# Kernel tuning notes

Measured on AMD Instinct MI355X. Metric: run time of the kernel, lower is better.

The kernel has to match this reference:

```python
import jax, jax.numpy as jnp
import numpy as np

# (multiplicity, dim=2l+1) per irreducible field, for both input and output
RS = [(8, 1), (8, 3), (8, 5)]
SIZE = 3          # conv kernel spatial size
B_EL = 2          # radial basis elements per (i,j) kernel block
EPS = 1e-5


def _se3_bn_conv(x, weight, bases):
    """Training-mode SE3BatchNorm stats fused into dynamic kernel build + conv3d.
    x: (B, C_in, D, H, W); weight: flat (sum mi*mj*b_el,);
    bases[i][j]: (b_el, di, dj, SIZE, SIZE, SIZE).
    """
    B = x.shape[0]
    means = []    # per scalar (d==1) field: (m,)
    scales = []   # per field: (m,) inverse-std factors
    ix = 0
    for m, d in RS:
        field = x[:, ix:ix + m * d].reshape(B, m, d, -1)
        ix += m * d
        if d == 1:
            mean = jax.lax.stop_gradient(field.mean(axis=-1).mean(axis=0).reshape(-1))
            field = field - mean.reshape(1, m, 1, 1)
            means.append(mean)
        # reduce='mean': sum over d, mean over spatial, mean over batch (detached)
        norm = jax.lax.stop_gradient(jnp.sum(field * field, axis=2).mean(axis=-1).mean(axis=0))
        scales.append((norm + EPS) ** -0.5)

    # Build normalized dynamic kernel blocks and compensating bias
    widx = 0
    row_blocks = []
    bias_parts = []
    for i, (mi, di) in enumerate(RS):
        col_blocks = []
        bia = jnp.zeros((mi * di,), x.dtype)
        imean = 0
        for j, (mj, dj) in enumerate(RS):
            basis = bases[i][j]                     # (b, di, dj, s, s, s)
            b = basis.shape[0]
            w = weight[widx:widx + mi * mj * b].reshape(mi, mj, b)
            widx += mi * mj * b
            w = w * scales[j][None, :, None]        # per-input-field BN rescale
            # block: (mi*di, mj*dj, s, s, s)
            block = jnp.einsum('uvb,bdexyz->udvexyz', w, basis)
            col_blocks.append(block.reshape(mi * di, mj * dj, SIZE, SIZE, SIZE))
            if di == 1 and dj == 1:
                mean = means[imean]
                imean += 1
                identity = basis.reshape(b, -1).sum(-1)         # (b,)
                corr = (w.reshape(-1, b) @ identity[:, None]).reshape(mi, mj)
                bia = bia - (corr @ mean[:, None]).reshape(-1)
        row_blocks.append(jnp.concatenate(col_blocks, axis=1))
        bias_parts.append(bia)
    kernel = jnp.concatenate(row_blocks, axis=0)    # (C_out, C_in, s, s, s)
    bias = jnp.concatenate(bias_parts)              # (C_out,)

    out = jax.lax.conv_general_dilated(
        x, kernel, window_strides=(1, 1, 1), padding='VALID',
        dimension_numbers=('NCDHW', 'OIDHW', 'NCDHW'))
    return out + bias[None, :, None, None, None]


def setup_inputs() -> dict:
    key = jax.random.key(0)
    k_x, k_w = jax.random.split(key)
    C = sum(m * d for m, d in RS)  # 72
    x = jax.random.normal(k_x, (8, C, 32, 32, 32), jnp.float32)
    total_w = sum(mi * mj * B_EL for mi, _ in RS for mj, _ in RS)  # 1152
    weight = jax.random.normal(k_w, (total_w,), jnp.float32) * 0.1
    inp = {'x': x, 'weight': weight}
    for i, (mi, di) in enumerate(RS):
        for j, (mj, dj) in enumerate(RS):
            kb = jax.random.fold_in(key, 100 + 10 * i + j)
            inp['basis_{}_{}'.format(i, j)] = jax.random.normal(
                kb, (B_EL, di, dj, SIZE, SIZE, SIZE), jnp.float32) / (SIZE ** 1.5)
    return inp


def reference(x, weight, basis_0_0, basis_0_1, basis_0_2,
              basis_1_0, basis_1_1, basis_1_2,
              basis_2_0, basis_2_1, basis_2_2):
    bases = [[basis_0_0, basis_0_1, basis_0_2],
             [basis_1_0, basis_1_1, basis_1_2],
             [basis_2_0, basis_2_1, basis_2_2]]
    return _se3_bn_conv(x, weight, bases)
```

## Files before the change

kernel.cpp:

```cpp
#include <hip/hip_runtime.h>
#include <hip/hip_fp16.h>
#include <math.h>

#define NCH 72
#define SP  32768
#define NBATCH 8
#define NTOT (NBATCH*SP)

#define WS_SUMX   0
#define WS_SUMSQ  72
#define WS_SCALE  144
#define WS_BIAS   216
#define WS_K      288

#define WS_XH_BYTES 323712
#define XH_ROW   2720
#define XH_PLANE 87040
#define XH_BATCH 2785280

typedef __attribute__((ext_vector_type(8))) _Float16 half8;
typedef __attribute__((ext_vector_type(4))) float float4v;
typedef __attribute__((ext_vector_type(4))) int int4v;

__device__ __forceinline__ void chmap(int c, int& f, int& m, int& d, int& dim) {
  if (c < 8)       { f = 0; m = c;          d = 0;          dim = 1; }
  else if (c < 32) { f = 1; m = (c - 8)/3;  d = (c - 8)%3;  dim = 3; }
  else             { f = 2; m = (c - 32)/5; d = (c - 32)%5; dim = 5; }
}

__global__ __launch_bounds__(256) void prepack_kernel(const float* __restrict__ x,
                                                      float* __restrict__ ws) {
  __shared__ __align__(16) short tile[256 * 88];
  __shared__ float segS[72][3], segQ[72][3];
  const int t    = threadIdx.x;
  const int z    = blockIdx.x >> 1;
  const int half = blockIdx.x & 1;
  const int b    = blockIdx.y;
  ushort* xh = (ushort*)((char*)ws + WS_XH_BYTES);
  const float* xb = x + (size_t)b * NCH * SP + z * 1024 + half * 512;

  const int ci_s = t % 72, seg = t / 72;
  float accS = 0.f, accQ = 0.f;

  *(int4v*)&tile[t * 88 + 72] = (int4v){0, 0, 0, 0};

  for (int c = 0; c < 2; ++c) {
    if (c) __syncthreads();
    #pragma unroll
    for (int cig = 0; cig < 18; ++cig) {
      float v0 = xb[(size_t)(cig*4 + 0) * SP + c * 256 + t];
      float v1 = xb[(size_t)(cig*4 + 1) * SP + c * 256 + t];
      float v2 = xb[(size_t)(cig*4 + 2) * SP + c * 256 + t];
      float v3 = xb[(size_t)(cig*4 + 3) * SP + c * 256 + t];
      short s4[4] = { (short)__half_as_short(__float2half(v0)),
                      (short)__half_as_short(__float2half(v1)),
                      (short)__half_as_short(__float2half(v2)),
                      (short)__half_as_short(__float2half(v3)) };
      *(int2*)&tile[t * 88 + cig * 4] = *(const int2*)s4;
    }
    __syncthreads();
    {
      ushort* gb = xh + (size_t)b * XH_BATCH + (size_t)(z * 32 + (half * 2 + c) * 8) * XH_ROW;
      #pragma unroll
      for (int j = 0; j < 10; ++j) {
        const int s   = t + j * 256;
        const int pos = s / 10, part = s - pos * 10;
        const int4v v = *(const int4v*)&tile[pos * 88 + part * 8];
        const int row = pos >> 5, xx = pos & 31;
        *(int4v*)(gb + (size_t)row * XH_ROW + xx * 80 + part * 8) = v;
      }
    }
    if (seg < 3) {
      const int p0 = seg * 86;
      const int pn = (seg == 2) ? 84 : 86;
      for (int i = 0; i < pn; ++i) {
        const float v = __half2float(__short_as_half(tile[(p0 + i) * 88 + ci_s]));
        accS += v; accQ += v * v;
      }
    }
  }
  if (seg < 3) { segS[ci_s][seg] = accS; segQ[ci_s][seg] = accQ; }
  __syncthreads();
  if (t < 144) {
    const int which = t / 72, ci = t % 72;
    const float v = which ? (segQ[ci][0] + segQ[ci][1] + segQ[ci][2])
                          : (segS[ci][0] + segS[ci][1] + segS[ci][2]);
    atomicAdd(&ws[(which ? WS_SUMSQ : WS_SUMX) + ci], v);
  }
}

__global__ __launch_bounds__(256) void build_half_kernel(const float* __restrict__ weight,
    float* __restrict__ ws,
    const float* __restrict__ b00, const float* __restrict__ b01, const float* __restrict__ b02,
    const float* __restrict__ b10, const float* __restrict__ b11, const float* __restrict__ b12,
    const float* __restrict__ b20, const float* __restrict__ b21, const float* __restrict__ b22) {
  const int tid = blockIdx.x * 256 + threadIdx.x;
  const float invN = 1.0f / (float)NTOT;
  if (tid < 315 * 512) {
    const int blk = tid >> 9;
    const int e   = tid & 511;
    const int tap = blk / 35;
    const int r   = blk - tap * 35;
    const int kc  = r / 5, cj = r - (r / 5) * 5;
    const int l   = e >> 3, j = e & 7;
    const int co  = cj * 16 + (l & 15);
    const int kk  = kc * 32 + ((l >> 4) << 3) + j;
    short val = 0;
    if (co < NCH && kk < 216) {
      const int dx = kk / 72, ci = kk - dx * 72;
      int fi, u, dd, di; chmap(co, fi, u, dd, di);
      int fj, v, ee, dj; chmap(ci, fj, v, ee, dj);
      const float* bs[9] = {b00, b01, b02, b10, b11, b12, b20, b21, b22};
      const float* basis = bs[fi * 3 + fj];
      float norm;
      if (ci < 8) {
        float m = ws[WS_SUMX + ci] * invN;
        norm = ws[WS_SUMSQ + ci] * invN - m * m;
      } else if (ci < 32) {
        int m0 = 8 + ((ci - 8) / 3) * 3;
        norm = (ws[WS_SUMSQ+m0] + ws[WS_SUMSQ+m0+1] + ws[WS_SUMSQ+m0+2]) * invN;
      } else {
        int m0 = 32 + ((ci - 32) / 5) * 5;
        norm = (ws[WS_SUMSQ+m0] + ws[WS_SUMSQ+m0+1] + ws[WS_SUMSQ+m0+2]
              + ws[WS_SUMSQ+m0+3] + ws[WS_SUMSQ+m0+4]) * invN;
      }
      const float sc = 1.0f / sqrtf(norm + 1e-5f);
      const float* wp = weight + (fi * 3 + fj) * 128 + (u * 8 + v) * 2;
      const float w0 = wp[0] * sc, w1 = wp[1] * sc;
      const int t = tap * 3 + dx;
      const float f = w0 * basis[(dd * dj + ee) * 27 + t]
                    + w1 * basis[((di + dd) * dj + ee) * 27 + t];
      val = __half_as_short(__float2half(f));
    }
    ((short*)(ws + WS_K))[tid] = val;
  }
  if (blockIdx.x == 0) {
    __shared__ float s_mean[8], s_scale[8];
    const int c = threadIdx.x;
    if (c < 8) {
      float m = ws[WS_SUMX + c] * invN;
      float norm = ws[WS_SUMSQ + c] * invN - m * m;
      s_mean[c]  = m;
      s_scale[c] = 1.0f / sqrtf(norm + 1e-5f);
    }
    __syncthreads();
    if (c < NCH) {
      float bia = 0.f;
      if (c < 8) {
        float id0 = 0.f, id1 = 0.f;
        #pragma unroll
        for (int t = 0; t < 27; ++t) { id0 += b00[t]; id1 += b00[27 + t]; }
        #pragma unroll
        for (int v = 0; v < 8; ++v) {
          float s  = s_scale[v];
          float w0 = weight[(c*8 + v)*2 + 0] * s;
          float w1 = weight[(c*8 + v)*2 + 1] * s;
          bia -= (w0 * id0 + w1 * id1) * s_mean[v];
        }
      }
      ws[WS_BIAS + c] = bia;
    }
  }
}

__global__ __launch_bounds__(128, 2) void conv_direct(const float* __restrict__ ws,
                                                      float* __restrict__ out) {
  const int lane = threadIdx.x & 63;
  const int wv   = threadIdx.x >> 6;
  const int lx   = lane & 15;
  const int q    = lane >> 4;
  const int i  = blockIdx.x;
  const int b  = i & 7;
  const int qq = i >> 3;
  const int yp = qq % 15;
  const int zp = qq / 15;
  const int y  = yp * 2 + wv;
  const int zb = zp * 2;

  const char* xhb = (const char*)ws + WS_XH_BYTES + (size_t)b * (XH_BATCH * 2);
  const char* Kb  = (const char*)(ws + WS_K);
  const float* __restrict__ bias = ws + WS_BIAS;

  const int lb16 = lane * 16;

  float4v acc[2][2][5];
  #pragma unroll
  for (int sz = 0; sz < 2; ++sz)
    #pragma unroll
    for (int s = 0; s < 2; ++s)
      #pragma unroll
      for (int cj = 0; cj < 5; ++cj)
        acc[sz][s][cj] = (float4v){0.f, 0.f, 0.f, 0.f};

#define LOADG(T, A, Bf) {                                                         \
    const int t_   = (T);                                                         \
    const int tap_ = t_ / 7;                                                      \
    const int kc_  = t_ - tap_ * 7;                                               \
    const int dz_  = tap_ / 3, dy_ = tap_ - 3 * dz_;                              \
    const char* r0_ = xhb + (size_t)(((zb + dz_) * 32) + (y + dy_)) * (XH_ROW*2); \
    const char* r1_ = r0_ + (XH_PLANE * 2);                                       \
    const char* bk_ = Kb + (size_t)tap_ * (35*1024) + (size_t)kc_ * (5*1024) + lb16; \
    const int kk0_ = kc_ * 32 + (q << 3);                                         \
    const int dx_  = (kk0_ >= 144) ? 2 : ((kk0_ >= 72) ? 1 : 0);                  \
    const int ao_  = (lx * 80 + kk0_ + 8 * dx_) * 2;                              \
    Bf[0] = *(const half8*)(bk_);                                                 \
    Bf[1] = *(const half8*)(bk_ + 1024);                                          \
    Bf[2] = *(const half8*)(bk_ + 2048);                                          \
    Bf[3] = *(const half8*)(bk_ + 3072);                                          \
    Bf[4] = *(const half8*)(bk_ + 4096);                                          \
    A[0] = *(const half8*)(r0_ + ao_);                                            \
    A[1] = *(const half8*)(r0_ + ao_ + 2560);                                     \
    A[2] = *(const half8*)(r1_ + ao_);                                            \
    A[3] = *(const half8*)(r1_ + ao_ + 2560);                                     \
  }

#define MF1(A, Bf, CJ)                                                                         \
    acc[0][0][CJ] = __builtin_amdgcn_mfma_f32_16x16x32_f16(A[0], Bf[CJ], acc[0][0][CJ], 0,0,0); \
    acc[0][1][CJ] = __builtin_amdgcn_mfma_f32_16x16x32_f16(A[1], Bf[CJ], acc[0][1][CJ], 0,0,0); \
    acc[1][0][CJ] = __builtin_amdgcn_mfma_f32_16x16x32_f16(A[2], Bf[CJ], acc[1][0][CJ], 0,0,0); \
    acc[1][1][CJ] = __builtin_amdgcn_mfma_f32_16x16x32_f16(A[3], Bf[CJ], acc[1][1][CJ], 0,0,0);

#define MFMAG(A, Bf) {                       \
    __builtin_amdgcn_s_setprio(1);           \
    MF1(A, Bf, 0) MF1(A, Bf, 1)              \
    MF1(A, Bf, 2) MF1(A, Bf, 3)              \
    MF1(A, Bf, 4)                            \
    __builtin_amdgcn_s_setprio(0);           \
  }

  half8 A0[4], B0[5], A1[4], B1[5], A2[4], B2[5];
  LOADG(0, A0, B0);
  LOADG(1, A1, B1);
  #pragma unroll 1
  for (int t = 0; t < 60; t += 3) {
    LOADG(t + 2, A2, B2);
    MFMAG(A0, B0);
    LOADG(t + 3, A0, B0);
    MFMAG(A1, B1);
    LOADG(t + 4, A1, B1);
    MFMAG(A2, B2);
  }
  LOADG(62, A2, B2);
  MFMAG(A0, B0);
  MFMAG(A1, B1);
  MFMAG(A2, B2);

#undef LOADG
#undef MF1
#undef MFMAG

  #pragma unroll
  for (int cj = 0; cj < 5; ++cj) {
    const int co = cj * 16 + lx;
    if (co < NCH) {
      const float bv = bias[co];
      #pragma unroll
      for (int sz = 0; sz < 2; ++sz) {
        float* ob = out + ((size_t)(b * NCH + co) * 30 + (zb + sz)) * 900 + y * 30;
        #pragma unroll
        for (int s = 0; s < 2; ++s) {
          const int x0 = s * 16 + q * 4;
          const float4v v = acc[sz][s][cj];
          float2 p0; p0.x = v[0] + bv; p0.y = v[1] + bv;
          *(float2*)(ob + x0) = p0;
          if (x0 + 2 < 30) {
            float2 p1; p1.x = v[2] + bv; p1.y = v[3] + bv;
            *(float2*)(ob + x0 + 2) = p1;
          }
        }
      }
    }
  }
}

extern "C" void kernel_launch(void* const* d_in, const int* in_sizes, int n_in,
                              void* d_out, int out_size, void* d_ws, size_t ws_size,
                              hipStream_t stream) {
  const float* x = (const float*)d_in[0];
  const float* w = (const float*)d_in[1];
  const float* bs[9];
  for (int i = 0; i < 9; ++i) bs[i] = (const float*)d_in[2 + i];
  float* ws  = (float*)d_ws;
  float* out = (float*)d_out;

  hipMemsetAsync(d_ws, 0, 144 * sizeof(float), stream);

  prepack_kernel<<<dim3(64, NBATCH), 256, 0, stream>>>(x, ws);
  build_half_kernel<<<(315 * 512 + 255) / 256, 256, 0, stream>>>(
      w, ws, bs[0], bs[1], bs[2], bs[3], bs[4], bs[5], bs[6], bs[7], bs[8]);
  conv_direct<<<dim3(1800), 128, 0, stream>>>(ws, out);
}
```

Measured before the change: 281.0 us.

## Stage per-tap weight tiles in LDS shared by four waves per block

The conv kernel now uses 256-thread blocks, each covering four y rows instead of two. For each of the nine taps, the block copies that tap's weight tile into shared memory with global_load_lds, and all four waves then read B fragments from LDS instead of each wave loading them from global memory. This cuts redundant global/L2 traffic for the weights. The cost is a barrier per tap and a padded y tile: y values past 29 are clamped and their outputs discarded, which wastes some MFMA work. The grid shrinks from 1800 to 960 blocks.

After: 255.9 us. 8.9% less time.

```diff
diff --git a/kernel.cpp b/kernel.cpp
--- a/kernel.cpp
+++ b/kernel.cpp
@@ -163,18 +163,21 @@
   }
 }
 
-__global__ __launch_bounds__(128, 2) void conv_direct(const float* __restrict__ ws,
+__global__ __launch_bounds__(256, 2) void conv_direct(const float* __restrict__ ws,
                                                       float* __restrict__ out) {
+  __shared__ __align__(16) char Bsm[35840];
+
   const int lane = threadIdx.x & 63;
   const int wv   = threadIdx.x >> 6;
   const int lx   = lane & 15;
   const int q    = lane >> 4;
   const int i  = blockIdx.x;
   const int b  = i & 7;
-  const int qq = i >> 3;
-  const int yp = qq % 15;
-  const int zp = qq / 15;
-  const int y  = yp * 2 + wv;
+  const int q2 = i >> 3;
+  const int yt = q2 & 7;
+  const int zp = q2 >> 3;
+  const int y  = yt * 4 + wv;
+  const int yc = (y > 29) ? 29 : y;
   const int zb = zp * 2;
 
   const char* xhb = (const char*)ws + WS_XH_BYTES + (size_t)b * (XH_BATCH * 2);
@@ -192,80 +195,98 @@
       for (int cj = 0; cj < 5; ++cj)
         acc[sz][s][cj] = (float4v){0.f, 0.f, 0.f, 0.f};
 
-#define LOADG(T, A, Bf) {                                                         \
-    const int t_   = (T);                                                         \
-    const int tap_ = t_ / 7;                                                      \
-    const int kc_  = t_ - tap_ * 7;                                               \
-    const int dz_  = tap_ / 3, dy_ = tap_ - 3 * dz_;                              \
-    const char* r0_ = xhb + (size_t)(((zb + dz_) * 32) + (y + dy_)) * (XH_ROW*2); \
-    const char* r1_ = r0_ + (XH_PLANE * 2);                                       \
-    const char* bk_ = Kb + (size_t)tap_ * (35*1024) + (size_t)kc_ * (5*1024) + lb16; \
-    const int kk0_ = kc_ * 32 + (q << 3);                                         \
+#define STAGE(TAP) {                                                              \
+    const char* src_ = Kb + (size_t)(TAP) * 35840;                                \
+    _Pragma("unroll")                                                             \
+    for (int k = 0; k < 9; ++k) {                                                 \
+      const int idx = (int)threadIdx.x + (k << 8);                                \
+      if (idx < 2240) {                                                           \
+        __builtin_amdgcn_global_load_lds(                                         \
+          (const __attribute__((address_space(1))) void*)(src_ + (size_t)idx*16), \
+          (__attribute__((address_space(3))) void*)(Bsm + ((k<<8) + (wv<<6))*16), \
+          16, 0, 0);                                                              \
+      }                                                                           \
+    }                                                                             \
+  }
+
+#define LOADA(KC, A) {                                                            \
+    const int kk0_ = (KC) * 32 + (q << 3);                                        \
     const int dx_  = (kk0_ >= 144) ? 2 : ((kk0_ >= 72) ? 1 : 0);                  \
     const int ao_  = (lx * 80 + kk0_ + 8 * dx_) * 2;                              \
-    Bf[0] = *(const half8*)(bk_);                                                 \
-    Bf[1] = *(const half8*)(bk_ + 1024);                                          \
-    Bf[2] = *(const half8*)(bk_ + 2048);                                          \
-    Bf[3] = *(const half8*)(bk_ + 3072);                                          \
-    Bf[4] = *(const half8*)(bk_ + 4096);                                          \
-    A[0] = *(const half8*)(r0_ + ao_);                                            \
-    A[1] = *(const half8*)(r0_ + ao_ + 2560);                                     \
-    A[2] = *(const half8*)(r1_ + ao_);                                            \
-    A[3] = *(const half8*)(r1_ + ao_ + 2560);                                     \
-  }
-
-#define MF1(A, Bf, CJ)                                                                         \
-    acc[0][0][CJ] = __builtin_amdgcn_mfma_f32_16x16x32_f16(A[0], Bf[CJ], acc[0][0][CJ], 0,0,0); \
-    acc[0][1][CJ] = __builtin_amdgcn_mfma_f32_16x16x32_f16(A[1], Bf[CJ], acc[0][1][CJ], 0,0,0); \
-    acc[1][0][CJ] = __builtin_amdgcn_mfma_f32_16x16x32_f16(A[2], Bf[CJ], acc[1][0][CJ], 0,0,0); \
-    acc[1][1][CJ] = __builtin_amdgcn_mfma_f32_16x16x32_f16(A[3], Bf[CJ], acc[1][1][CJ], 0,0,0);
-
-#define MFMAG(A, Bf) {                       \
-    __builtin_amdgcn_s_setprio(1);           \
-    MF1(A, Bf, 0) MF1(A, Bf, 1)              \
-    MF1(A, Bf, 2) MF1(A, Bf, 3)              \
-    MF1(A, Bf, 4)                            \
-    __builtin_amdgcn_s_setprio(0);           \
-  }
-
-  half8 A0[4], B0[5], A1[4], B1[5], A2[4], B2[5];
-  LOADG(0, A0, B0);
-  LOADG(1, A1, B1);
+    A[0] = *(const half8*)(r0T + ao_);                                            \
+    A[1] = *(const half8*)(r0T + ao_ + 2560);                                     \
+    A[2] = *(const half8*)(r1T + ao_);                                            \
+    A[3] = *(const half8*)(r1T + ao_ + 2560);                                     \
+  }
+
+#define MFQ(A, BF, CJ)                                                                         \
+    acc[0][0][CJ] = __builtin_amdgcn_mfma_f32_16x16x32_f16(A[0], BF, acc[0][0][CJ], 0,0,0);    \
+    acc[0][1][CJ] = __builtin_amdgcn_mfma_f32_16x16x32_f16(A[1], BF, acc[0][1][CJ], 0,0,0);    \
+    acc[1][0][CJ] = __builtin_amdgcn_mfma_f32_16x16x32_f16(A[2], BF, acc[1][0][CJ], 0,0,0);    \
+    acc[1][1][CJ] = __builtin_amdgcn_mfma_f32_16x16x32_f16(A[3], BF, acc[1][1][CJ], 0,0,0);
+
+#define GROUP(KC, AC, PRE) {                                                      \
+    half8 bf0 = *(const half8*)(Bsm + ((KC)*5 + 0)*1024 + lb16);                  \
+    half8 bf1 = *(const half8*)(Bsm + ((KC)*5 + 1)*1024 + lb16);                  \
+    half8 bf2 = *(const half8*)(Bsm + ((KC)*5 + 2)*1024 + lb16);                  \
+    half8 bf3 = *(const half8*)(Bsm + ((KC)*5 + 3)*1024 + lb16);                  \
+    half8 bf4 = *(const half8*)(Bsm + ((KC)*5 + 4)*1024 + lb16);                  \
+    PRE;                                                                          \
+    __builtin_amdgcn_s_setprio(1);                                                \
+    MFQ(AC, bf0, 0) MFQ(AC, bf1, 1) MFQ(AC, bf2, 2) MFQ(AC, bf3, 3) MFQ(AC, bf4, 4) \
+    __builtin_amdgcn_s_setprio(0);                                                \
+  }
+
+  half8 A0[4], A1[4], A2[4];
+
   #pragma unroll 1
-  for (int t = 0; t < 60; t += 3) {
-    LOADG(t + 2, A2, B2);
-    MFMAG(A0, B0);
-    LOADG(t + 3, A0, B0);
-    MFMAG(A1, B1);
-    LOADG(t + 4, A1, B1);
-    MFMAG(A2, B2);
-  }
-  LOADG(62, A2, B2);
-  MFMAG(A0, B0);
-  MFMAG(A1, B1);
-  MFMAG(A2, B2);
-
-#undef LOADG
-#undef MF1
-#undef MFMAG
-
-  #pragma unroll
-  for (int cj = 0; cj < 5; ++cj) {
-    const int co = cj * 16 + lx;
-    if (co < NCH) {
-      const float bv = bias[co];
-      #pragma unroll
-      for (int sz = 0; sz < 2; ++sz) {
-        float* ob = out + ((size_t)(b * NCH + co) * 30 + (zb + sz)) * 900 + y * 30;
+  for (int tap = 0; tap < 9; ++tap) {
+    const int dz_ = tap / 3, dy_ = tap - dz_ * 3;
+    const char* r0T = xhb + (size_t)(((zb + dz_) * 32) + (yc + dy_)) * (XH_ROW * 2);
+    const char* r1T = r0T + (XH_PLANE * 2);
+
+    if (tap) __builtin_amdgcn_s_barrier();
+    STAGE(tap);
+    __builtin_amdgcn_sched_barrier(0);
+    LOADA(0, A0); LOADA(1, A1);
+    __builtin_amdgcn_sched_barrier(0);
+    asm volatile("s_waitcnt vmcnt(8)" ::: "memory");
+    __builtin_amdgcn_s_barrier();
+    __builtin_amdgcn_sched_barrier(0);
+
+    GROUP(0, A0, LOADA(2, A2));
+    GROUP(1, A1, LOADA(3, A0));
+    GROUP(2, A2, LOADA(4, A1));
+    GROUP(3, A0, LOADA(5, A2));
+    GROUP(4, A1, LOADA(6, A0));
+    GROUP(5, A2, (void)0);
+    GROUP(6, A0, (void)0);
+  }
+
+#undef STAGE
+#undef LOADA
+#undef MFQ
+#undef GROUP
+
+  if (y < 30) {
+    #pragma unroll
+    for (int cj = 0; cj < 5; ++cj) {
+      const int co = cj * 16 + lx;
+      if (co < NCH) {
+        const float bv = bias[co];
         #pragma unroll
-        for (int s = 0; s < 2; ++s) {
-          const int x0 = s * 16 + q * 4;
-          const float4v v = acc[sz][s][cj];
-          float2 p0; p0.x = v[0] + bv; p0.y = v[1] + bv;
-          *(float2*)(ob + x0) = p0;
-          if (x0 + 2 < 30) {
-            float2 p1; p1.x = v[2] + bv; p1.y = v[3] + bv;
-            *(float2*)(ob + x0 + 2) = p1;
+        for (int sz = 0; sz < 2; ++sz) {
+          float* ob = out + ((size_t)(b * NCH + co) * 30 + (zb + sz)) * 900 + y * 30;
+          #pragma unroll
+          for (int s = 0; s < 2; ++s) {
+            const int x0 = s * 16 + q * 4;
+            const float4v v = acc[sz][s][cj];
+            float2 p0; p0.x = v[0] + bv; p0.y = v[1] + bv;
+            *(float2*)(ob + x0) = p0;
+            if (x0 + 2 < 30) {
+              float2 p1; p1.x = v[2] + bv; p1.y = v[3] + bv;
+              *(float2*)(ob + x0 + 2) = p1;
+            }
           }
         }
       }
@@ -288,5 +309,5 @@
   prepack_kernel<<<dim3(64, NBATCH), 256, 0, stream>>>(x, ws);
   build_half_kernel<<<(315 * 512 + 255) / 256, 256, 0, stream>>>(
       w, ws, bs[0], bs[1], bs[2], bs[3], bs[4], bs[5], bs[6], bs[7], bs[8]);
-  conv_direct<<<dim3(1800), 128, 0, stream>>>(ws, out);
-}
+  conv_direct<<<dim3(960), 256, 0, stream>>>(ws, out);
+}
```
